# Kernel tuning notes

Measured on AMD Instinct MI355X. Metric: run time of the kernel, lower is better.

Reference implementation:

```python
import jax, jax.numpy as jnp
import numpy as np

DROPOUT_P = 0.5
INV_SCALE = 1.0
_DROP_KEY = jax.random.key(42)


def setup_inputs() -> dict:
    key = jax.random.key(0)
    kq, kk, kv = jax.random.split(key, 3)
    B, H, S, D = 4, 16, 2048, 64
    return {
        "query": jax.random.normal(kq, (B, H, S, D), dtype=jnp.float32),
        "key": jax.random.normal(kk, (B, H, S, D), dtype=jnp.float32),
        "value": jax.random.normal(kv, (B, H, S, D), dtype=jnp.float32),
    }


def reference(query, key, value):
    # qk = Q @ K^T, scaled, softmax over last axis
    qk = jnp.einsum("bhqd,bhkd->bhqk", query, key) / INV_SCALE
    p = jax.nn.softmax(qk, axis=-1)
    # inverted dropout with a fixed RNG key (deterministic reference)
    keep = jax.random.bernoulli(_DROP_KEY, 1.0 - DROPOUT_P, p.shape)
    p = jnp.where(keep, p / (1.0 - DROPOUT_P), 0.0)
    # attention output: P @ V
    return jnp.einsum("bhqk,bhkd->bhqd", p, value)
```

## Files before the change

kernel.cpp:

```cpp
#include <hip/hip_runtime.h>


#define S_LEN 2048
#define D_DIM 64
#define KT    32
#define QT    16
#define NWAVE 4
#define KSTR  72
#define VROW  66
#define PSTR  40

typedef short  short8  __attribute__((ext_vector_type(8)));
typedef float  floatx4 __attribute__((ext_vector_type(4)));

__device__ __forceinline__ unsigned rotl(unsigned x, int r) {
  return __builtin_amdgcn_alignbit(x, x, 32 - r);
}

__device__ __forceinline__ unsigned drop_mask(unsigned i) {
  const unsigned KS1 = 42u;
  const unsigned KS2 = 0x1BD11BDAu ^ 42u;
  unsigned a = 0u;
  unsigned b = i + KS1;
#define TFR(r) { a += b; b = rotl(b, r); b ^= a; }
  TFR(13) TFR(15) TFR(26) TFR(6)   a += KS1; b += KS2 + 1u;
  TFR(17) TFR(29) TFR(16) TFR(24)  a += KS2; b += 2u;
  TFR(13) TFR(15) TFR(26) TFR(6)             b += KS1 + 3u;
  TFR(17) TFR(29) TFR(16) TFR(24)  a += KS1; b += KS2 + 4u;
  TFR(13) TFR(15) TFR(26) TFR(6)   a += KS2; b += 5u;
#undef TFR
  return (unsigned)(((int)(a ^ b)) >> 31);
}

__device__ __forceinline__ void split_bf16(float x, unsigned short& h, unsigned short& l) {
  unsigned u = __float_as_uint(x);
  h = (unsigned short)(u >> 16);
  float r = x - __uint_as_float(u & 0xFFFF0000u);
  l = (unsigned short)(__float_as_uint(r) >> 16);
}

#define MFMA(a, b, c) __builtin_amdgcn_mfma_f32_16x16x32_bf16((a), (b), (c), 0, 0, 0)

__global__ __launch_bounds__(256, 6) void attn_fused_v7(
    const float* __restrict__ Qg, const float* __restrict__ Kg,
    const float* __restrict__ Vg, float* __restrict__ Og) {

  __shared__ __attribute__((aligned(16))) unsigned short Kh[KT * KSTR];
  __shared__ __attribute__((aligned(16))) unsigned short Kl[KT * KSTR];
  __shared__ __attribute__((aligned(16))) unsigned short Vs[KT * VROW];
  __shared__ __attribute__((aligned(16))) unsigned short Ph[NWAVE][QT * PSTR];

  const int tid  = threadIdx.x;
  const int wave = tid >> 6;
  const int lane = tid & 63;
  const int m16  = lane & 15;
  const int quad = lane >> 4;

  const int bh    = blockIdx.x >> 5;
  const int qtile = blockIdx.x & 31;
  const int q0    = qtile * (QT * NWAVE) + wave * QT;
  const size_t head_off = (size_t)bh * S_LEN * D_DIM;

  short8 qh[2], ql[2];
#pragma unroll
  for (int kc = 0; kc < 2; ++kc) {
    const float* qp = Qg + head_off + (size_t)(q0 + m16) * D_DIM + kc * 32 + quad * 8;
    floatx4 f0 = *(const floatx4*)qp;
    floatx4 f1 = *(const floatx4*)(qp + 4);
#pragma unroll
    for (int e = 0; e < 4; ++e) {
      unsigned short h, l;
      split_bf16(f0[e], h, l);
      qh[kc][e] = (short)h;  ql[kc][e] = (short)l;
      split_bf16(f1[e], h, l);
      qh[kc][4 + e] = (short)h;  ql[kc][4 + e] = (short)l;
    }
  }

  floatx4 o_acc[4];
#pragma unroll
  for (int n = 0; n < 4; ++n) o_acc[n] = (floatx4){0.f, 0.f, 0.f, 0.f};
  float lsum[4];
#pragma unroll
  for (int r = 0; r < 4; ++r) lsum[r] = 0.f;

  const unsigned ibase0 =
      ((unsigned)(bh * S_LEN + q0 + quad * 4)) * (unsigned)S_LEN + (unsigned)m16;

  const int srow = tid >> 4;
  const int sc4  = (tid & 15) << 2;
  const float* kbase = Kg + head_off + (size_t)srow * D_DIM + sc4;
  const float* vbase = Vg + head_off + (size_t)srow * D_DIM + sc4;

  floatx4 kpre0 = *(const floatx4*)(kbase);
  floatx4 kpre1 = *(const floatx4*)(kbase + 16 * D_DIM);
  floatx4 vpre0 = *(const floatx4*)(vbase);
  floatx4 vpre1 = *(const floatx4*)(vbase + 16 * D_DIM);

  for (int kb = 0; kb < S_LEN; kb += KT) {
    asm volatile("s_waitcnt lgkmcnt(0)" ::: "memory");
    __builtin_amdgcn_s_barrier();

#pragma unroll
    for (int half = 0; half < 2; ++half) {
      floatx4 kv = half ? kpre1 : kpre0;
      floatx4 vv = half ? vpre1 : vpre0;
      int row = srow + half * 16;
      unsigned short h0, h1, h2, h3, l0, l1, l2, l3;
      split_bf16(kv[0], h0, l0); split_bf16(kv[1], h1, l1);
      split_bf16(kv[2], h2, l2); split_bf16(kv[3], h3, l3);
      int kidx = row * KSTR + sc4;
      *(unsigned*)&Kh[kidx]     = (unsigned)h0 | ((unsigned)h1 << 16);
      *(unsigned*)&Kh[kidx + 2] = (unsigned)h2 | ((unsigned)h3 << 16);
      *(unsigned*)&Kl[kidx]     = (unsigned)l0 | ((unsigned)l1 << 16);
      *(unsigned*)&Kl[kidx + 2] = (unsigned)l2 | ((unsigned)l3 << 16);
      unsigned v01 = (__float_as_uint(vv[0]) >> 16) |
                     (__float_as_uint(vv[1]) & 0xFFFF0000u);
      unsigned v23 = (__float_as_uint(vv[2]) >> 16) |
                     (__float_as_uint(vv[3]) & 0xFFFF0000u);
      int vidx = row * VROW + sc4;
      *(unsigned*)&Vs[vidx]     = v01;
      *(unsigned*)&Vs[vidx + 2] = v23;
    }

    if (kb + KT < S_LEN) {
      const float* kp = kbase + (size_t)(kb + KT) * D_DIM;
      const float* vp = vbase + (size_t)(kb + KT) * D_DIM;
      kpre0 = *(const floatx4*)(kp);
      kpre1 = *(const floatx4*)(kp + 16 * D_DIM);
      vpre0 = *(const floatx4*)(vp);
      vpre1 = *(const floatx4*)(vp + 16 * D_DIM);
    }

    asm volatile("s_waitcnt lgkmcnt(0)" ::: "memory");
    __builtin_amdgcn_s_barrier();

    floatx4 sc[2];
#pragma unroll
    for (int nb = 0; nb < 2; ++nb) {
      floatx4 acc = (floatx4){0.f, 0.f, 0.f, 0.f};
#pragma unroll
      for (int kc = 0; kc < 2; ++kc) {
        int bidx = (nb * 16 + m16) * KSTR + kc * 32 + quad * 8;
        short8 kbh = *(const short8*)&Kh[bidx];
        short8 kbl = *(const short8*)&Kl[bidx];
        acc = MFMA(qh[kc], kbh, acc);
        acc = MFMA(qh[kc], kbl, acc);
        acc = MFMA(ql[kc], kbh, acc);
      }
      sc[nb] = acc;
    }

#pragma unroll
    for (int nb = 0; nb < 2; ++nb)
#pragma unroll
      for (int r = 0; r < 4; ++r) {
        float pe = __expf(sc[nb][r]);
        lsum[r] += pe;
        unsigned i = ibase0 + (unsigned)kb + (unsigned)(r * S_LEN) + (unsigned)(nb * 16);
        unsigned hbits = (__float_as_uint(pe) >> 16) & ~drop_mask(i);
        Ph[wave][(quad * 4 + r) * PSTR + nb * 16 + m16] = (unsigned short)hbits;
      }

    short8 pa = *(const short8*)&Ph[wave][m16 * PSTR + quad * 8];
#pragma unroll
    for (int n = 0; n < 4; ++n) {
      short8 vb;
#pragma unroll
      for (int j = 0; j < 8; ++j)
        vb[j] = (short)Vs[(quad * 8 + j) * VROW + n * 16 + m16];
      o_acc[n] = MFMA(pa, vb, o_acc[n]);
    }
  }

#pragma unroll
  for (int off = 8; off >= 1; off >>= 1)
#pragma unroll
    for (int r = 0; r < 4; ++r)
      lsum[r] += __shfl_xor(lsum[r], off, 64);

#pragma unroll
  for (int r = 0; r < 4; ++r) {
    float scale = 2.0f / lsum[r];
#pragma unroll
    for (int n = 0; n < 4; ++n) {
      Og[head_off + (size_t)(q0 + quad * 4 + r) * D_DIM + n * 16 + m16] =
          o_acc[n][r] * scale;
    }
  }
}

extern "C" void kernel_launch(void* const* d_in, const int* in_sizes, int n_in,
                              void* d_out, int out_size, void* d_ws, size_t ws_size,
                              hipStream_t stream) {
  (void)in_sizes; (void)n_in; (void)out_size; (void)d_ws; (void)ws_size;
  const float* Q = (const float*)d_in[0];
  const float* K = (const float*)d_in[1];
  const float* V = (const float*)d_in[2];
  float* O = (float*)d_out;
  hipLaunchKernelGGL(attn_fused_v7, dim3(2048), dim3(256), 0, stream, Q, K, V, O);
}
```

Before: 883.8 us.

## Hand-schedule dropout Threefry in inline asm and drop K/V register prefetch

Replaces the C++ Threefry dropout-mask function with an inline-asm routine that computes two counters interleaved. It folds the first round algebraically because a starts at zero, and uses alignbit rotations and constant adds directly. The aim is to cut VALU instruction count and dependency stalls in the RNG, which dominates per-tile work. It also removes the register double-buffered K/V prefetch in favour of direct loads inside the tile loop with plain __syncthreads. That lowers register pressure but exposes global-load latency each iteration. The rotation constants are rewritten as right-shift amounts, so correctness depends on matching the reference bit pattern exactly.

```diff
diff --git a/kernel.cpp b/kernel.cpp
--- a/kernel.cpp
+++ b/kernel.cpp
@@ -13,23 +13,53 @@
 typedef short  short8  __attribute__((ext_vector_type(8)));
 typedef float  floatx4 __attribute__((ext_vector_type(4)));
 
-__device__ __forceinline__ unsigned rotl(unsigned x, int r) {
-  return __builtin_amdgcn_alignbit(x, x, 32 - r);
-}
-
-__device__ __forceinline__ unsigned drop_mask(unsigned i) {
-  const unsigned KS1 = 42u;
-  const unsigned KS2 = 0x1BD11BDAu ^ 42u;
-  unsigned a = 0u;
-  unsigned b = i + KS1;
-#define TFR(r) { a += b; b = rotl(b, r); b ^= a; }
-  TFR(13) TFR(15) TFR(26) TFR(6)   a += KS1; b += KS2 + 1u;
-  TFR(17) TFR(29) TFR(16) TFR(24)  a += KS2; b += 2u;
-  TFR(13) TFR(15) TFR(26) TFR(6)             b += KS1 + 3u;
-  TFR(17) TFR(29) TFR(16) TFR(24)  a += KS1; b += KS2 + 4u;
-  TFR(13) TFR(15) TFR(26) TFR(6)   a += KS2; b += 5u;
-#undef TFR
-  return (unsigned)(((int)(a ^ b)) >> 31);
+#define TF_R2(sh) \
+  "v_add_u32 %1, %1, %0\n\t" \
+  "v_add_u32 %3, %3, %2\n\t" \
+  "v_alignbit_b32 %0, %0, %0, " #sh "\n\t" \
+  "v_alignbit_b32 %2, %2, %2, " #sh "\n\t" \
+  "v_xor_b32 %0, %0, %1\n\t" \
+  "v_xor_b32 %2, %2, %3\n\t"
+
+__device__ __forceinline__ void tf2(unsigned i0, unsigned i1,
+                                    unsigned& w0, unsigned& w1) {
+  unsigned a0, a1;
+  asm(
+    "v_add_u32 %0, 42, %4\n\t"
+    "v_add_u32 %2, 42, %5\n\t"
+    "v_mov_b32 %1, %0\n\t"
+    "v_mov_b32 %3, %2\n\t"
+    "v_alignbit_b32 %0, %0, %0, 19\n\t"
+    "v_alignbit_b32 %2, %2, %2, 19\n\t"
+    "v_xor_b32 %0, %0, %1\n\t"
+    "v_xor_b32 %2, %2, %3\n\t"
+    TF_R2(17) TF_R2(6) TF_R2(26)
+    "v_add_u32 %1, 42, %1\n\t"
+    "v_add_u32 %3, 42, %3\n\t"
+    "v_add_u32 %0, 0x1bd11bf1, %0\n\t"
+    "v_add_u32 %2, 0x1bd11bf1, %2\n\t"
+    TF_R2(15) TF_R2(3) TF_R2(16) TF_R2(8)
+    "v_add_u32 %1, 0x1bd11bf0, %1\n\t"
+    "v_add_u32 %3, 0x1bd11bf0, %3\n\t"
+    "v_add_u32 %0, 2, %0\n\t"
+    "v_add_u32 %2, 2, %2\n\t"
+    TF_R2(19) TF_R2(17) TF_R2(6) TF_R2(26)
+    "v_add_u32 %0, 45, %0\n\t"
+    "v_add_u32 %2, 45, %2\n\t"
+    TF_R2(15) TF_R2(3) TF_R2(16) TF_R2(8)
+    "v_add_u32 %1, 42, %1\n\t"
+    "v_add_u32 %3, 42, %3\n\t"
+    "v_add_u32 %0, 0x1bd11bf4, %0\n\t"
+    "v_add_u32 %2, 0x1bd11bf4, %2\n\t"
+    TF_R2(19) TF_R2(17) TF_R2(6) TF_R2(26)
+    "v_add_u32 %1, 0x1bd11bf0, %1\n\t"
+    "v_add_u32 %3, 0x1bd11bf0, %3\n\t"
+    "v_add_u32 %0, 5, %0\n\t"
+    "v_add_u32 %2, 5, %2\n\t"
+    "v_xor_b32 %0, %0, %1\n\t"
+    "v_xor_b32 %2, %2, %3"
+    : "=&v"(w0), "=&v"(a0), "=&v"(w1), "=&v"(a1)
+    : "v"(i0), "v"(i1));
 }
 
 __device__ __forceinline__ void split_bf16(float x, unsigned short& h, unsigned short& l) {
@@ -41,7 +71,7 @@
 
 #define MFMA(a, b, c) __builtin_amdgcn_mfma_f32_16x16x32_bf16((a), (b), (c), 0, 0, 0)
 
-__global__ __launch_bounds__(256, 6) void attn_fused_v7(
+__global__ __launch_bounds__(256, 6) void attn_fused_v10(
     const float* __restrict__ Qg, const float* __restrict__ Kg,
     const float* __restrict__ Vg, float* __restrict__ Og) {
 
@@ -87,29 +117,19 @@
   const unsigned ibase0 =
       ((unsigned)(bh * S_LEN + q0 + quad * 4)) * (unsigned)S_LEN + (unsigned)m16;
 
-  const int srow = tid >> 4;
-  const int sc4  = (tid & 15) << 2;
-  const float* kbase = Kg + head_off + (size_t)srow * D_DIM + sc4;
-  const float* vbase = Vg + head_off + (size_t)srow * D_DIM + sc4;
-
-  floatx4 kpre0 = *(const floatx4*)(kbase);
-  floatx4 kpre1 = *(const floatx4*)(kbase + 16 * D_DIM);
-  floatx4 vpre0 = *(const floatx4*)(vbase);
-  floatx4 vpre1 = *(const floatx4*)(vbase + 16 * D_DIM);
-
   for (int kb = 0; kb < S_LEN; kb += KT) {
-    asm volatile("s_waitcnt lgkmcnt(0)" ::: "memory");
-    __builtin_amdgcn_s_barrier();
-
-#pragma unroll
-    for (int half = 0; half < 2; ++half) {
-      floatx4 kv = half ? kpre1 : kpre0;
-      floatx4 vv = half ? vpre1 : vpre0;
-      int row = srow + half * 16;
+    __syncthreads();
+
+    for (int f = tid; f < KT * (D_DIM / 4); f += 256) {
+      int row = f >> 4;
+      int c4  = (f & 15) << 2;
+      size_t goff = head_off + (size_t)(kb + row) * D_DIM + c4;
+      floatx4 kv = *(const floatx4*)(Kg + goff);
+      floatx4 vv = *(const floatx4*)(Vg + goff);
       unsigned short h0, h1, h2, h3, l0, l1, l2, l3;
       split_bf16(kv[0], h0, l0); split_bf16(kv[1], h1, l1);
       split_bf16(kv[2], h2, l2); split_bf16(kv[3], h3, l3);
-      int kidx = row * KSTR + sc4;
+      int kidx = row * KSTR + c4;
       *(unsigned*)&Kh[kidx]     = (unsigned)h0 | ((unsigned)h1 << 16);
       *(unsigned*)&Kh[kidx + 2] = (unsigned)h2 | ((unsigned)h3 << 16);
       *(unsigned*)&Kl[kidx]     = (unsigned)l0 | ((unsigned)l1 << 16);
@@ -118,22 +138,11 @@
                      (__float_as_uint(vv[1]) & 0xFFFF0000u);
       unsigned v23 = (__float_as_uint(vv[2]) >> 16) |
                      (__float_as_uint(vv[3]) & 0xFFFF0000u);
-      int vidx = row * VROW + sc4;
+      int vidx = row * VROW + c4;
       *(unsigned*)&Vs[vidx]     = v01;
       *(unsigned*)&Vs[vidx + 2] = v23;
     }
-
-    if (kb + KT < S_LEN) {
-      const float* kp = kbase + (size_t)(kb + KT) * D_DIM;
-      const float* vp = vbase + (size_t)(kb + KT) * D_DIM;
-      kpre0 = *(const floatx4*)(kp);
-      kpre1 = *(const floatx4*)(kp + 16 * D_DIM);
-      vpre0 = *(const floatx4*)(vp);
-      vpre1 = *(const floatx4*)(vp + 16 * D_DIM);
-    }
-
-    asm volatile("s_waitcnt lgkmcnt(0)" ::: "memory");
-    __builtin_amdgcn_s_barrier();
+    __syncthreads();
 
     floatx4 sc[2];
 #pragma unroll
@@ -152,15 +161,20 @@
     }
 
 #pragma unroll
-    for (int nb = 0; nb < 2; ++nb)
-#pragma unroll
-      for (int r = 0; r < 4; ++r) {
+    for (int r = 0; r < 4; ++r) {
+      unsigned i0 = ibase0 + (unsigned)kb + (unsigned)(r * S_LEN);
+      unsigned w0, w1;
+      tf2(i0, i0 + 16u, w0, w1);
+#pragma unroll
+      for (int nb = 0; nb < 2; ++nb) {
         float pe = __expf(sc[nb][r]);
         lsum[r] += pe;
-        unsigned i = ibase0 + (unsigned)kb + (unsigned)(r * S_LEN) + (unsigned)(nb * 16);
-        unsigned hbits = (__float_as_uint(pe) >> 16) & ~drop_mask(i);
+        unsigned hbits = __float_as_uint(pe) >> 16;
+        unsigned w = nb ? w1 : w0;
+        hbits = ((int)w < 0) ? 0u : hbits;
         Ph[wave][(quad * 4 + r) * PSTR + nb * 16 + m16] = (unsigned short)hbits;
       }
+    }
 
     short8 pa = *(const short8*)&Ph[wave][m16 * PSTR + quad * 8];
 #pragma unroll
@@ -198,5 +212,5 @@
   const float* K = (const float*)d_in[1];
   const float* V = (const float*)d_in[2];
   float* O = (float*)d_out;
-  hipLaunchKernelGGL(attn_fused_v7, dim3(2048), dim3(256), 0, stream, Q, K, V, O);
-}
+  hipLaunchKernelGGL(attn_fused_v10, dim3(2048), dim3(256), 0, stream, Q, K, V, O);
+}
```

New measurement: 799.7 us. 9.5% less time.
